# Performance work log

Hardware: AMD Instinct MI355X
Metric: run time of the kernel (lower is better)

Reference implementation:

```python
import jax, jax.numpy as jnp
import numpy as np

N = 500_000   # raw points
S = 10_000    # superpoints
D = 256       # feature dim
HID = 1024    # MLP hidden = 4*D
K = 10        # sampled raw points per superpoint (code default)


def setup_inputs() -> dict:
    key = jax.random.key(0)
    k1, k2, k3, k4, k5 = jax.random.split(key, 5)
    raw_feats = jax.random.normal(k1, (N, D), dtype=jnp.float32)
    sp_idx = jax.random.randint(k2, (N,), 0, S)
    rand_idx = jax.random.randint(k3, (S, K), 0, K)
    w1 = jax.random.normal(k4, (D, HID), dtype=jnp.float32) * (1.0 / np.sqrt(D))
    b1 = jnp.zeros((HID,), dtype=jnp.float32)
    w2 = jax.random.normal(k5, (HID, D), dtype=jnp.float32) * (1.0 / np.sqrt(HID))
    b2 = jnp.zeros((D,), dtype=jnp.float32)
    return {
        "raw_feats": raw_feats, "w1": w1, "b1": b1, "w2": w2, "b2": b2,
        "sp_idx": sp_idx, "rand_idx": rand_idx, "n_superpoints": S,
    }


def reference(raw_feats, w1, b1, w2, b2, sp_idx, rand_idx, n_superpoints):
    S_ = int(n_superpoints)
    n = raw_feats.shape[0]

    # --- average_pool_by_sp: segment-mean of point features per superpoint ---
    sums = jax.ops.segment_sum(raw_feats, sp_idx, num_segments=S_)          # (S, D)
    cnt = jax.ops.segment_sum(jnp.ones((n,), raw_feats.dtype), sp_idx,
                              num_segments=S_)                              # (S,)
    x_sp = sums / jnp.maximum(cnt, 1.0)[:, None]                            # (S, D)

    # --- build_sp_sequences_tensor: sort points by sp, modular random gather ---
    order = jnp.argsort(sp_idx)                 # stable sort, like torch.argsort
    sorted_feats = raw_feats[order]             # (N, D)
    counts = cnt.astype(jnp.int32)              # (S,) points per superpoint
    starts = jnp.concatenate([jnp.zeros((1,), jnp.int32),
                              jnp.cumsum(counts)[:-1]])                     # (S,) exclusive cumsum
    max_len = jnp.maximum(counts, 1)
    gather_idx = starts[:, None] + (rand_idx.astype(jnp.int32) % max_len[:, None])  # (S, K)
    sampled = sorted_feats[gather_idx]          # (S, K, D)
    seq = jnp.concatenate([sampled, x_sp[:, None, :]], axis=1)              # (S, K+1, D)

    # --- MLP over sequence tokens: fc1 -> GELU -> fc2 ---
    h = jax.nn.gelu(jnp.einsum('skd,dh->skh', seq, w1) + b1)
    out = jnp.einsum('skh,hd->skd', h, w2) + b2                             # (S, K+1, D)
    return out
```

## Files before the change

### kernel.cpp

```cpp
#include <hip/hip_runtime.h>
#include <hip/hip_bf16.h>

typedef __attribute__((ext_vector_type(8))) short short8;
typedef __attribute__((ext_vector_type(4))) float f32x4;

__device__ __forceinline__ unsigned short f2bf(float f){
  __hip_bfloat16 h = __float2bfloat16(f);
  return *reinterpret_cast<unsigned short*>(&h);
}

__device__ __forceinline__ float gelu_t(float x){
  float u = 0.7978845608028654f * (x + 0.044715f * x * x * x);
  float e = __expf(2.0f * u);
  float t = 1.0f - 2.0f / (e + 1.0f);
  return 0.5f * x * (1.0f + t);
}

__global__ void k_hist(const int* __restrict__ sp, int* __restrict__ cnt, int N){
  int i = blockIdx.x * blockDim.x + threadIdx.x;
  if (i < N) atomicAdd(&cnt[sp[i]], 1);
}

__global__ void k_scan(const int* __restrict__ cnt, int* __restrict__ starts, int S){
  __shared__ int part[256];
  int tid = threadIdx.x;
  int chunk = (S + 255) / 256;
  int lo = tid * chunk;
  int hi = min(lo + chunk, S);
  int sum = 0;
  for (int i = lo; i < hi; i++) sum += cnt[i];
  part[tid] = sum;
  __syncthreads();
  if (tid == 0){
    int run = 0;
    for (int i = 0; i < 256; i++){ int v = part[i]; part[i] = run; run += v; }
  }
  __syncthreads();
  int run = part[tid];
  for (int i = lo; i < hi; i++){ starts[i] = run; run += cnt[i]; }
}

__global__ void k_scatter(const int* __restrict__ sp, const int* __restrict__ starts,
                          int* __restrict__ fill, int* __restrict__ perm, int N){
  int i = blockIdx.x * blockDim.x + threadIdx.x;
  if (i < N){
    int s = sp[i];
    int pos = atomicAdd(&fill[s], 1);
    perm[starts[s] + pos] = i;
  }
}

#define MAXC 512
__global__ void k_rank(const int* __restrict__ perm, const int* __restrict__ starts,
                       const int* __restrict__ cnt, int* __restrict__ perm2, int S){
  __shared__ int buf[4][MAXC];
  int wv = threadIdx.x >> 6;
  int lane = threadIdx.x & 63;
  int s = blockIdx.x * 4 + wv;
  int st = 0, c = 0;
  if (s < S){ st = starts[s]; c = cnt[s]; }
  if (c <= MAXC){
    for (int j = lane; j < c; j += 64) buf[wv][j] = perm[st + j];
  }
  __syncthreads();
  if (c <= MAXC){
    for (int j = lane; j < c; j += 64){
      int v = buf[wv][j];
      int r = 0;
      for (int m = 0; m < c; m++) r += (buf[wv][m] < v) ? 1 : 0;
      perm2[st + r] = v;
    }
  } else {
    for (int j = lane; j < c; j += 64) perm2[st + j] = perm[st + j];
  }
}

__global__ void k_pool(const float* __restrict__ raw, const int* __restrict__ perm,
                       const int* __restrict__ starts, const int* __restrict__ cnt,
                       float* __restrict__ xsp){
  __shared__ float red[4][64][4];
  int s = blockIdx.x;
  int lane = threadIdx.x & 63;
  int wv = threadIdx.x >> 6;
  int st = starts[s], c = cnt[s];
  float4 acc = make_float4(0.f, 0.f, 0.f, 0.f);
  for (int m = wv; m < c; m += 4){
    int r = perm[st + m];
    float4 v = reinterpret_cast<const float4*>(raw)[(size_t)r * 64 + lane];
    acc.x += v.x; acc.y += v.y; acc.z += v.z; acc.w += v.w;
  }
  red[wv][lane][0] = acc.x; red[wv][lane][1] = acc.y;
  red[wv][lane][2] = acc.z; red[wv][lane][3] = acc.w;
  __syncthreads();
  if (wv == 0){
    float inv = 1.0f / (float)max(c, 1);
    float4 o;
    o.x = (red[0][lane][0] + red[1][lane][0] + red[2][lane][0] + red[3][lane][0]) * inv;
    o.y = (red[0][lane][1] + red[1][lane][1] + red[2][lane][1] + red[3][lane][1]) * inv;
    o.z = (red[0][lane][2] + red[1][lane][2] + red[2][lane][2] + red[3][lane][2]) * inv;
    o.w = (red[0][lane][3] + red[1][lane][3] + red[2][lane][3] + red[3][lane][3]) * inv;
    reinterpret_cast<float4*>(xsp)[(size_t)s * 64 + lane] = o;
  }
}

__global__ void k_castT(const float* __restrict__ in, unsigned short* __restrict__ out,
                        int A, int B){
  int i = blockIdx.x * blockDim.x + threadIdx.x;
  if (i >= A * B) return;
  int b = i / A, a = i - b * A;
  out[(size_t)b * A + a] = f2bf(in[(size_t)a * B + b]);
}

__global__ void k_seq(const float* __restrict__ raw, const float* __restrict__ xsp,
                      const int* __restrict__ perm2, const int* __restrict__ starts,
                      const int* __restrict__ cnt, const int* __restrict__ rnd,
                      unsigned short* __restrict__ seq, int S, int K, int N, int D){
  int t = blockIdx.x;
  int lane = threadIdx.x;
  int kp1 = K + 1;
  int s = t / kp1;
  int j = t - s * kp1;
  const float* src;
  if (j < K){
    int c = cnt[s];
    int ml = max(c, 1);
    int gi = starts[s] + (rnd[s * K + j] % ml);
    gi = min(gi, N - 1);
    src = raw + (size_t)perm2[gi] * D;
  } else {
    src = xsp + (size_t)s * D;
  }
  float4 v = reinterpret_cast<const float4*>(src)[lane];
  ushort4 o;
  o.x = f2bf(v.x); o.y = f2bf(v.y); o.z = f2bf(v.z); o.w = f2bf(v.w);
  reinterpret_cast<ushort4*>(seq + (size_t)t * D)[lane] = o;
}

__global__ __launch_bounds__(512, 4)
void k_mlp(const unsigned short* __restrict__ seq, const unsigned short* __restrict__ w1t,
           const unsigned short* __restrict__ w2t, const float* __restrict__ bias1,
           const float* __restrict__ bias2, float* __restrict__ out, int Ttot){
  extern __shared__ char ldsraw[];
  unsigned short* seq_lds = (unsigned short*)ldsraw;
  unsigned short* w1_lds  = seq_lds + 64 * 256;
  unsigned short* h_lds   = w1_lds + 64 * 256;

  const int tid  = threadIdx.x;
  const int lane = tid & 63;
  const int wv   = tid >> 6;
  const int tg   = wv & 3;
  const int hh   = wv >> 2;
  const int l15  = lane & 15;
  const int lhi  = lane >> 4;
  const int t0   = blockIdx.x * 64;

  #pragma unroll
  for (int rpt = 0; rpt < 4; rpt++){
    int idx = rpt * 512 + tid;
    int row = idx >> 5, gr = idx & 31;
    int t = t0 + row;
    int4 v = make_int4(0, 0, 0, 0);
    if (t < Ttot) v = *reinterpret_cast<const int4*>(seq + (size_t)t * 256 + gr * 8);
    *reinterpret_cast<int4*>(seq_lds + row * 256 + ((gr ^ (row & 7)) << 3)) = v;
  }

  f32x4 acc2[4][2];
  #pragma unroll
  for (int rf = 0; rf < 4; rf++)
    #pragma unroll
    for (int cf = 0; cf < 2; cf++) acc2[rf][cf] = (f32x4){0.f, 0.f, 0.f, 0.f};

  for (int c = 0; c < 16; c++){
    __syncthreads();

    #pragma unroll
    for (int rpt = 0; rpt < 4; rpt++){
      int idx = rpt * 512 + tid;
      int row = idx >> 5, gr = idx & 31;
      int4 v = *reinterpret_cast<const int4*>(w1t + (size_t)(c * 64 + row) * 256 + gr * 8);
      *reinterpret_cast<int4*>(w1_lds + row * 256 + ((gr ^ (row & 7)) << 3)) = v;
    }

    short8 w2f[2][2];
    #pragma unroll
    for (int cf = 0; cf < 2; cf++)
      #pragma unroll
      for (int ks = 0; ks < 2; ks++)
        w2f[cf][ks] = *reinterpret_cast<const short8*>(
            w2t + (size_t)(wv * 32 + cf * 16 + l15) * 1024 + c * 64 + ks * 32 + lhi * 8);
    float bv1[2];
    bv1[0] = bias1[c * 64 + hh * 32 + l15];
    bv1[1] = bias1[c * 64 + hh * 32 + 16 + l15];

    __syncthreads();

    f32x4 acc1[2];
    acc1[0] = (f32x4){0.f, 0.f, 0.f, 0.f};
    acc1[1] = (f32x4){0.f, 0.f, 0.f, 0.f};
    const int arow = tg * 16 + l15;
    #pragma unroll
    for (int ks = 0; ks < 8; ks++){
      int agr = (ks * 4 + lhi) ^ (arow & 7);
      short8 a = *reinterpret_cast<const short8*>(seq_lds + arow * 256 + agr * 8);
      #pragma unroll
      for (int fc = 0; fc < 2; fc++){
        int brow = hh * 32 + fc * 16 + l15;
        int bgr = (ks * 4 + lhi) ^ (brow & 7);
        short8 b = *reinterpret_cast<const short8*>(w1_lds + brow * 256 + bgr * 8);
        acc1[fc] = __builtin_amdgcn_mfma_f32_16x16x32_bf16(a, b, acc1[fc], 0, 0, 0);
      }
    }
    #pragma unroll
    for (int fc = 0; fc < 2; fc++){
      int col = hh * 32 + fc * 16 + l15;
      #pragma unroll
      for (int q = 0; q < 4; q++){
        int row = tg * 16 + lhi * 4 + q;
        float v = acc1[fc][q] + bv1[fc];
        int phys = (col >> 3) ^ (row & 7);
        h_lds[row * 64 + phys * 8 + (col & 7)] = f2bf(gelu_t(v));
      }
    }
    __syncthreads();

    #pragma unroll
    for (int ks = 0; ks < 2; ks++){
      short8 af[4];
      #pragma unroll
      for (int rf = 0; rf < 4; rf++){
        int hrow = rf * 16 + l15;
        int hgr = (ks * 4 + lhi) ^ (hrow & 7);
        af[rf] = *reinterpret_cast<const short8*>(h_lds + hrow * 64 + hgr * 8);
      }
      #pragma unroll
      for (int cf = 0; cf < 2; cf++)
        #pragma unroll
        for (int rf = 0; rf < 4; rf++)
          acc2[rf][cf] = __builtin_amdgcn_mfma_f32_16x16x32_bf16(af[rf], w2f[cf][ks],
                                                                 acc2[rf][cf], 0, 0, 0);
    }
  }

  #pragma unroll
  for (int cf = 0; cf < 2; cf++){
    int dcol = wv * 32 + cf * 16 + l15;
    float bv = bias2[dcol];
    #pragma unroll
    for (int rf = 0; rf < 4; rf++){
      #pragma unroll
      for (int q = 0; q < 4; q++){
        int t = t0 + rf * 16 + lhi * 4 + q;
        if (t < Ttot) out[(size_t)t * 256 + dcol] = acc2[rf][cf][q] + bv;
      }
    }
  }
}

extern "C" void kernel_launch(void* const* d_in, const int* in_sizes, int n_in,
                              void* d_out, int out_size, void* d_ws, size_t ws_size,
                              hipStream_t stream){
  const float* raw = (const float*)d_in[0];
  const float* w1  = (const float*)d_in[1];
  const float* b1  = (const float*)d_in[2];
  const float* w2  = (const float*)d_in[3];
  const float* b2  = (const float*)d_in[4];
  const int* sp    = (const int*)d_in[5];
  const int* rnd   = (const int*)d_in[6];

  const int N    = in_sizes[5];
  const int D    = in_sizes[0] / N;
  const int HID  = in_sizes[2];
  const int SK   = in_sizes[6];
  const int Ttot = out_size / D;
  const int S    = Ttot - SK;
  const int K    = SK / S;

  char* ws = (char*)d_ws;
  size_t off = 0;
  auto alloc = [&](size_t bytes) -> char* {
    char* p = ws + off;
    off += (bytes + 255) & ~(size_t)255;
    return p;
  };
  int* cnt    = (int*)alloc((size_t)S * 4);
  int* fill   = (int*)alloc((size_t)S * 4);
  int* starts = (int*)alloc((size_t)S * 4);
  int* perm   = (int*)alloc((size_t)N * 4);
  int* perm2  = (int*)alloc((size_t)N * 4);
  float* xsp  = (float*)alloc((size_t)S * D * 4);
  unsigned short* w1t = (unsigned short*)alloc((size_t)D * HID * 2);
  unsigned short* w2t = (unsigned short*)alloc((size_t)HID * D * 2);
  unsigned short* seq = (unsigned short*)alloc((size_t)(S * (K + 1)) * D * 2);

  hipMemsetAsync(cnt, 0, (size_t)S * 4, stream);
  hipMemsetAsync(fill, 0, (size_t)S * 4, stream);

  int nb = (N + 255) / 256;
  k_hist<<<nb, 256, 0, stream>>>(sp, cnt, N);
  k_scan<<<1, 256, 0, stream>>>(cnt, starts, S);
  k_scatter<<<nb, 256, 0, stream>>>(sp, starts, fill, perm, N);
  k_rank<<<(S + 3) / 4, 256, 0, stream>>>(perm, starts, cnt, perm2, S);
  k_pool<<<S, 256, 0, stream>>>(raw, perm, starts, cnt, xsp);
  k_castT<<<(D * HID + 255) / 256, 256, 0, stream>>>(w1, w1t, D, HID);
  k_castT<<<(HID * D + 255) / 256, 256, 0, stream>>>(w2, w2t, HID, D);
  k_seq<<<Ttot, 64, 0, stream>>>(raw, xsp, perm2, starts, cnt, rnd, seq, S, K, N, D);

  int mlpBlocks = (Ttot + 63) / 64;
  size_t ldsBytes = (size_t)(64 * 256 + 64 * 256 + 64 * 64) * sizeof(unsigned short);
  hipFuncSetAttribute((const void*)k_mlp, hipFuncAttributeMaxDynamicSharedMemorySize,
                      (int)ldsBytes);
  k_mlp<<<mlpBlocks, 512, ldsBytes, stream>>>(seq, w1t, w2t, b1, b2, (float*)d_out, Ttot);
}
```

Before: 1.055 ms.

## Fuse pooling and sequence gather into one kernel, hoist MLP A fragments

Result: no change. 1.058 ms (+0.3%).

```diff
diff --git a/kernel.cpp b/kernel.cpp
--- a/kernel.cpp
+++ b/kernel.cpp
@@ -75,23 +75,61 @@
   }
 }
 
-__global__ void k_pool(const float* __restrict__ raw, const int* __restrict__ perm,
-                       const int* __restrict__ starts, const int* __restrict__ cnt,
-                       float* __restrict__ xsp){
+#define KMAX 16
+__global__ __launch_bounds__(256)
+void k_pool(const float* __restrict__ raw, const int* __restrict__ perm2,
+            const int* __restrict__ starts, const int* __restrict__ cnt,
+            const int* __restrict__ rnd, unsigned short* __restrict__ seq,
+            int S, int K, int N){
+  __shared__ int lidx[MAXC];
   __shared__ float red[4][64][4];
+  __shared__ int tgt[KMAX];
   int s = blockIdx.x;
-  int lane = threadIdx.x & 63;
-  int wv = threadIdx.x >> 6;
+  int tid = threadIdx.x;
+  int lane = tid & 63;
+  int wv = tid >> 6;
   int st = starts[s], c = cnt[s];
-  float4 acc = make_float4(0.f, 0.f, 0.f, 0.f);
-  for (int m = wv; m < c; m += 4){
-    int r = perm[st + m];
-    float4 v = reinterpret_cast<const float4*>(raw)[(size_t)r * 64 + lane];
-    acc.x += v.x; acc.y += v.y; acc.z += v.z; acc.w += v.w;
-  }
+  int cc = min(c, MAXC);
+
+  for (int m = tid; m < cc; m += 256) lidx[m] = perm2[st + m];
+  if (tid < K){
+    int ml = max(c, 1);
+    tgt[tid] = rnd[s * K + tid] % ml;
+  }
+  __syncthreads();
+
+  float4 a0 = {0,0,0,0}, a1 = {0,0,0,0}, a2 = {0,0,0,0}, a3 = {0,0,0,0};
+  const float4* rawv = reinterpret_cast<const float4*>(raw);
+  int m = wv;
+  for (; m + 12 < c; m += 16){
+    int i0 = (m      < MAXC) ? lidx[m]      : perm2[st + m];
+    int i1 = (m + 4  < MAXC) ? lidx[m + 4]  : perm2[st + m + 4];
+    int i2 = (m + 8  < MAXC) ? lidx[m + 8]  : perm2[st + m + 8];
+    int i3 = (m + 12 < MAXC) ? lidx[m + 12] : perm2[st + m + 12];
+    float4 v0 = rawv[(size_t)i0 * 64 + lane];
+    float4 v1 = rawv[(size_t)i1 * 64 + lane];
+    float4 v2 = rawv[(size_t)i2 * 64 + lane];
+    float4 v3 = rawv[(size_t)i3 * 64 + lane];
+    a0.x += v0.x; a0.y += v0.y; a0.z += v0.z; a0.w += v0.w;
+    a1.x += v1.x; a1.y += v1.y; a1.z += v1.z; a1.w += v1.w;
+    a2.x += v2.x; a2.y += v2.y; a2.z += v2.z; a2.w += v2.w;
+    a3.x += v3.x; a3.y += v3.y; a3.z += v3.z; a3.w += v3.w;
+  }
+  for (; m < c; m += 4){
+    int i0 = (m < MAXC) ? lidx[m] : perm2[st + m];
+    float4 v0 = rawv[(size_t)i0 * 64 + lane];
+    a0.x += v0.x; a0.y += v0.y; a0.z += v0.z; a0.w += v0.w;
+  }
+  float4 acc;
+  acc.x = (a0.x + a1.x) + (a2.x + a3.x);
+  acc.y = (a0.y + a1.y) + (a2.y + a3.y);
+  acc.z = (a0.z + a1.z) + (a2.z + a3.z);
+  acc.w = (a0.w + a1.w) + (a2.w + a3.w);
   red[wv][lane][0] = acc.x; red[wv][lane][1] = acc.y;
   red[wv][lane][2] = acc.z; red[wv][lane][3] = acc.w;
   __syncthreads();
+
+  size_t tokbase = (size_t)s * (K + 1);
   if (wv == 0){
     float inv = 1.0f / (float)max(c, 1);
     float4 o;
@@ -99,7 +137,20 @@
     o.y = (red[0][lane][1] + red[1][lane][1] + red[2][lane][1] + red[3][lane][1]) * inv;
     o.z = (red[0][lane][2] + red[1][lane][2] + red[2][lane][2] + red[3][lane][2]) * inv;
     o.w = (red[0][lane][3] + red[1][lane][3] + red[2][lane][3] + red[3][lane][3]) * inv;
-    reinterpret_cast<float4*>(xsp)[(size_t)s * 64 + lane] = o;
+    ushort4 ob;
+    ob.x = f2bf(o.x); ob.y = f2bf(o.y); ob.z = f2bf(o.z); ob.w = f2bf(o.w);
+    reinterpret_cast<ushort4*>(seq)[(tokbase + K) * 64 + lane] = ob;
+  }
+
+  for (int j = wv; j < K; j += 4){
+    int g = tgt[j];
+    int idx;
+    if (g < cc) idx = lidx[g];
+    else        idx = perm2[min(st + g, N - 1)];
+    float4 v = rawv[(size_t)idx * 64 + lane];
+    ushort4 o;
+    o.x = f2bf(v.x); o.y = f2bf(v.y); o.z = f2bf(v.z); o.w = f2bf(v.w);
+    reinterpret_cast<ushort4*>(seq)[(tokbase + j) * 64 + lane] = o;
   }
 }
 
@@ -109,31 +160,6 @@
   if (i >= A * B) return;
   int b = i / A, a = i - b * A;
   out[(size_t)b * A + a] = f2bf(in[(size_t)a * B + b]);
-}
-
-__global__ void k_seq(const float* __restrict__ raw, const float* __restrict__ xsp,
-                      const int* __restrict__ perm2, const int* __restrict__ starts,
-                      const int* __restrict__ cnt, const int* __restrict__ rnd,
-                      unsigned short* __restrict__ seq, int S, int K, int N, int D){
-  int t = blockIdx.x;
-  int lane = threadIdx.x;
-  int kp1 = K + 1;
-  int s = t / kp1;
-  int j = t - s * kp1;
-  const float* src;
-  if (j < K){
-    int c = cnt[s];
-    int ml = max(c, 1);
-    int gi = starts[s] + (rnd[s * K + j] % ml);
-    gi = min(gi, N - 1);
-    src = raw + (size_t)perm2[gi] * D;
-  } else {
-    src = xsp + (size_t)s * D;
-  }
-  float4 v = reinterpret_cast<const float4*>(src)[lane];
-  ushort4 o;
-  o.x = f2bf(v.x); o.y = f2bf(v.y); o.z = f2bf(v.z); o.w = f2bf(v.w);
-  reinterpret_cast<ushort4*>(seq + (size_t)t * D)[lane] = o;
 }
 
 __global__ __launch_bounds__(512, 4)
@@ -163,6 +189,15 @@
     if (t < Ttot) v = *reinterpret_cast<const int4*>(seq + (size_t)t * 256 + gr * 8);
     *reinterpret_cast<int4*>(seq_lds + row * 256 + ((gr ^ (row & 7)) << 3)) = v;
   }
+  __syncthreads();
+
+  short8 afrag[8];
+  const int arow = tg * 16 + l15;
+  #pragma unroll
+  for (int ks = 0; ks < 8; ks++){
+    int agr = (ks * 4 + lhi) ^ (arow & 7);
+    afrag[ks] = *reinterpret_cast<const short8*>(seq_lds + arow * 256 + agr * 8);
+  }
 
   f32x4 acc2[4][2];
   #pragma unroll
@@ -197,17 +232,14 @@
     f32x4 acc1[2];
     acc1[0] = (f32x4){0.f, 0.f, 0.f, 0.f};
     acc1[1] = (f32x4){0.f, 0.f, 0.f, 0.f};
-    const int arow = tg * 16 + l15;
     #pragma unroll
     for (int ks = 0; ks < 8; ks++){
-      int agr = (ks * 4 + lhi) ^ (arow & 7);
-      short8 a = *reinterpret_cast<const short8*>(seq_lds + arow * 256 + agr * 8);
       #pragma unroll
       for (int fc = 0; fc < 2; fc++){
         int brow = hh * 32 + fc * 16 + l15;
         int bgr = (ks * 4 + lhi) ^ (brow & 7);
         short8 b = *reinterpret_cast<const short8*>(w1_lds + brow * 256 + bgr * 8);
-        acc1[fc] = __builtin_amdgcn_mfma_f32_16x16x32_bf16(a, b, acc1[fc], 0, 0, 0);
+        acc1[fc] = __builtin_amdgcn_mfma_f32_16x16x32_bf16(afrag[ks], b, acc1[fc], 0, 0, 0);
       }
     }
     #pragma unroll
@@ -287,7 +319,6 @@
   int* starts = (int*)alloc((size_t)S * 4);
   int* perm   = (int*)alloc((size_t)N * 4);
   int* perm2  = (int*)alloc((size_t)N * 4);
-  float* xsp  = (float*)alloc((size_t)S * D * 4);
   unsigned short* w1t = (unsigned short*)alloc((size_t)D * HID * 2);
   unsigned short* w2t = (unsigned short*)alloc((size_t)HID * D * 2);
   unsigned short* seq = (unsigned short*)alloc((size_t)(S * (K + 1)) * D * 2);
@@ -300,10 +331,9 @@
   k_scan<<<1, 256, 0, stream>>>(cnt, starts, S);
   k_scatter<<<nb, 256, 0, stream>>>(sp, starts, fill, perm, N);
   k_rank<<<(S + 3) / 4, 256, 0, stream>>>(perm, starts, cnt, perm2, S);
-  k_pool<<<S, 256, 0, stream>>>(raw, perm, starts, cnt, xsp);
   k_castT<<<(D * HID + 255) / 256, 256, 0, stream>>>(w1, w1t, D, HID);
   k_castT<<<(HID * D + 255) / 256, 256, 0, stream>>>(w2, w2t, HID, D);
-  k_seq<<<Ttot, 64, 0, stream>>>(raw, xsp, perm2, starts, cnt, rnd, seq, S, K, N, D);
+  k_pool<<<S, 256, 0, stream>>>(raw, perm2, starts, cnt, rnd, seq, S, K, N);
 
   int mlpBlocks = (Ttot + 63) / 64;
   size_t ldsBytes = (size_t)(64 * 256 + 64 * 256 + 64 * 64) * sizeof(unsigned short);
```
